# Optimization experiments

Hardware: AMD Instinct MI355X
Metric: run time of the kernel (lower is better)

Reference implementation:

```python
import jax, jax.numpy as jnp
import numpy as np

N, E, F_IN, F_E, H, T = 100000, 1600000, 128, 16, 64, 32
NEG_SLOPE = 0.2


def setup_inputs() -> dict:
    key = jax.random.key(0)
    ks = jax.random.split(key, 24)
    s = 0.1
    inp = {
        'x': jax.random.normal(ks[0], (N, F_IN), jnp.float32),
        'edge_index': jax.random.randint(ks[1], (2, E), 0, N, dtype=jnp.int32),
        'edge_attr': jax.random.normal(ks[2], (E, F_E), jnp.float32),
        # GATConv layer 1 (heads=1)
        'W1': jax.random.normal(ks[3], (F_IN, H), jnp.float32) * s,
        'as1': jax.random.normal(ks[4], (H,), jnp.float32) * s,
        'ad1': jax.random.normal(ks[5], (H,), jnp.float32) * s,
        'We1': jax.random.normal(ks[6], (F_E, H), jnp.float32) * s,
        'ae1': jax.random.normal(ks[7], (H,), jnp.float32) * s,
        'b1': jnp.zeros((H,), jnp.float32),
        # GATConv layer 2
        'W2': jax.random.normal(ks[8], (H, H), jnp.float32) * s,
        'as2': jax.random.normal(ks[9], (H,), jnp.float32) * s,
        'ad2': jax.random.normal(ks[10], (H,), jnp.float32) * s,
        'We2': jax.random.normal(ks[11], (F_E, H), jnp.float32) * s,
        'ae2': jax.random.normal(ks[12], (H,), jnp.float32) * s,
        'b2': jnp.zeros((H,), jnp.float32),
        # classifier MLP (dropout in eval mode -> identity)
        'Wc1': jax.random.normal(ks[13], (H, H // 2), jnp.float32) * s,
        'bc1': jnp.zeros((H // 2,), jnp.float32),
        'Wc2': jax.random.normal(ks[14], (H // 2, T), jnp.float32) * s,
        'bc2': jnp.zeros((T,), jnp.float32),
    }
    return inp


def gat_conv(x, src, dst, edge_attr, W, a_s, a_d, We, a_e, b):
    """Single-head PyG-style GATConv with edge features and self-loops
    (self-loop edge_attr = mean of incoming edge_attr, fill_value='mean')."""
    n = x.shape[0]
    # self loops with mean incoming edge features
    deg = jax.ops.segment_sum(jnp.ones_like(dst, jnp.float32), dst, n)
    loop_attr = jax.ops.segment_sum(edge_attr, dst, n) / jnp.maximum(deg, 1.0)[:, None]
    loops = jnp.arange(n, dtype=src.dtype)
    src_f = jnp.concatenate([src, loops])
    dst_f = jnp.concatenate([dst, loops])
    ea = jnp.concatenate([edge_attr, loop_attr], axis=0)  # [E+N, F_E]
    h = x @ W                                             # [N, H]
    # attention logits per edge: alpha_src[j] + alpha_dst[i] + alpha_edge
    alpha = (h @ a_s)[src_f] + (h @ a_d)[dst_f] + (ea @ We) @ a_e
    alpha = jax.nn.leaky_relu(alpha, NEG_SLOPE)
    # segment softmax over incoming edges per destination node
    m = jax.ops.segment_max(alpha, dst_f, n)
    p = jnp.exp(alpha - m[dst_f])
    z = jax.ops.segment_sum(p, dst_f, n)
    w = p / z[dst_f]                                      # [E+N]
    out = jax.ops.segment_sum(w[:, None] * h[src_f], dst_f, n)
    return out + b


def reference(x, edge_index, edge_attr, W1, as1, ad1, We1, ae1, b1,
              W2, as2, ad2, We2, ae2, b2, Wc1, bc1, Wc2, bc2):
    src, dst = edge_index[0], edge_index[1]
    h = jax.nn.relu(gat_conv(x, src, dst, edge_attr, W1, as1, ad1, We1, ae1, b1))
    h = jax.nn.relu(gat_conv(h, src, dst, edge_attr, W2, as2, ad2, We2, ae2, b2))
    h = jax.nn.relu(h @ Wc1 + bc1)
    logits = h @ Wc2 + bc2
    return logits
```

## Files before the change

kernel.cpp:

```cpp
#include <hip/hip_runtime.h>
#include <hip/hip_bf16.h>
#include <hip/hip_fp16.h>

#define NEG_SLOPE 0.2f
#define EPB 2048
#define NBUK 512

__device__ __forceinline__ float leaky(float a) { return a > 0.f ? a : NEG_SLOPE * a; }

__global__ __launch_bounds__(256) void count_pack(
    const int* __restrict__ dst, const float* __restrict__ eattr,
    const float* __restrict__ We1, const float* __restrict__ ae1,
    const float* __restrict__ We2, const float* __restrict__ ae2,
    unsigned int* __restrict__ meta_pay, int* __restrict__ counts, int E) {
    __shared__ float wvs[32];
    __shared__ int hist[NBUK];
    int tid = threadIdx.x, i = blockIdx.x;
    if (tid < 32) {
        const float* Wp = (tid < 16) ? We1 : We2;
        const float* ap = (tid < 16) ? ae1 : ae2;
        int f = tid & 15;
        float s = 0.f;
        for (int k = 0; k < 64; ++k) s += Wp[f * 64 + k] * ap[k];
        wvs[tid] = s;
    }
    for (int t = tid; t < NBUK; t += 256) hist[t] = 0;
    __syncthreads();
    int e0 = i * EPB, e1 = min(E, e0 + EPB);
    for (int e = e0 + tid; e < e1; e += 256) {
        int d = dst[e];
        atomicAdd(&hist[d >> 8], 1);
        const float4* ep = (const float4*)(eattr + (size_t)e * 16);
        float4 q0 = ep[0], q1 = ep[1], q2 = ep[2], q3 = ep[3];
        float a[16] = {q0.x, q0.y, q0.z, q0.w, q1.x, q1.y, q1.z, q1.w,
                       q2.x, q2.y, q2.z, q2.w, q3.x, q3.y, q3.z, q3.w};
        float s1 = 0.f, s2 = 0.f;
#pragma unroll
        for (int f = 0; f < 16; ++f) { s1 += a[f] * wvs[f]; s2 += a[f] * wvs[16 + f]; }
        unsigned int p1 = (unsigned int)__half_as_ushort(__float2half_rn(s1));
        unsigned int p2 = (unsigned int)__half_as_ushort(__float2half_rn(s2));
        meta_pay[e] = p1 | (p2 << 16);
    }
    __syncthreads();
    for (int t = tid; t < NBUK; t += 256) counts[(size_t)i * NBUK + t] = hist[t];
}

__global__ __launch_bounds__(1024) void scan_cols(const int* __restrict__ counts,
                                                  int* __restrict__ offsets,
                                                  int* __restrict__ btot, int nblk) {
    __shared__ int sh[1024];
    int b = blockIdx.x, t = threadIdx.x;
    int v = (t < nblk) ? counts[(size_t)t * NBUK + b] : 0;
    sh[t] = v;
    __syncthreads();
    for (int off = 1; off < 1024; off <<= 1) {
        int u = (t >= off) ? sh[t - off] : 0;
        __syncthreads();
        sh[t] += u;
        __syncthreads();
    }
    if (t < nblk) offsets[(size_t)t * NBUK + b] = sh[t] - v;
    if (t == 1023) btot[b] = sh[1023];
}

__global__ void scan_buckets(const int* __restrict__ btot, int* __restrict__ bbase,
                             int* __restrict__ rowptr, int E, int n) {
    __shared__ int sh[NBUK];
    int t = threadIdx.x;
    int v = btot[t];
    sh[t] = v;
    __syncthreads();
    for (int off = 1; off < NBUK; off <<= 1) {
        int u = (t >= off) ? sh[t - off] : 0;
        __syncthreads();
        sh[t] += u;
        __syncthreads();
    }
    bbase[t] = sh[t] - v;
    if (t == 0) rowptr[n] = E;
}

__global__ __launch_bounds__(256) void scatter_buckets(
    const int* __restrict__ dst, const int* __restrict__ src,
    const unsigned int* __restrict__ meta_pay, const int* __restrict__ offsets,
    const int* __restrict__ bbase, uint2* __restrict__ bucketed, int E) {
    __shared__ int cur[NBUK];
    int i = blockIdx.x, tid = threadIdx.x;
    for (int t = tid; t < NBUK; t += 256) cur[t] = bbase[t] + offsets[(size_t)i * NBUK + t];
    __syncthreads();
    int e0 = i * EPB, e1 = min(E, e0 + EPB);
    for (int e = e0 + tid; e < e1; e += 256) {
        int d = dst[e];
        int slot = atomicAdd(&cur[d >> 8], 1);
        bucketed[slot] = make_uint2((unsigned int)src[e] | ((unsigned int)(d & 255) << 24),
                                    meta_pay[e]);
    }
}

__global__ __launch_bounds__(256) void csr_build(const uint2* __restrict__ bucketed,
                                                 const int* __restrict__ bbase,
                                                 const int* __restrict__ btot,
                                                 int* __restrict__ rowptr,
                                                 uint2* __restrict__ recs, int n) {
    __shared__ int deg[256], sc[256], cur[256];
    int b = blockIdx.x, tid = threadIdx.x;
    int base = bbase[b], cnt = btot[b];
    deg[tid] = 0;
    __syncthreads();
    for (int k = tid; k < cnt; k += 256) {
        uint2 r = bucketed[base + k];
        atomicAdd(&deg[r.x >> 24], 1);
    }
    __syncthreads();
    int dv = deg[tid];
    sc[tid] = dv;
    __syncthreads();
    for (int off = 1; off < 256; off <<= 1) {
        int u = (tid >= off) ? sc[tid - off] : 0;
        __syncthreads();
        sc[tid] += u;
        __syncthreads();
    }
    int excl = sc[tid] - dv;
    int d = b * 256 + tid;
    if (d < n) rowptr[d] = base + excl;
    cur[tid] = base + excl;
    __syncthreads();
    for (int k = tid; k < cnt; k += 256) {
        uint2 r = bucketed[base + k];
        int dl = (int)(r.x >> 24);
        int pos = atomicAdd(&cur[dl], 1);
        recs[pos] = make_uint2(r.x & 0x00FFFFFFu, r.y);
    }
}

template <int K>
__global__ __launch_bounds__(256) void gemm_node(const float* __restrict__ X,
                                                 const float* __restrict__ W,
                                                 const float* __restrict__ a_s,
                                                 const float* __restrict__ a_d,
                                                 __half* __restrict__ Hout16,
                                                 float* __restrict__ ash,
                                                 float* __restrict__ adh, int n) {
    constexpr int KC = 64;
    __shared__ float xs[128 * 65];
    __shared__ float ws[KC * 64];
    int tid = threadIdx.x;
    int base = blockIdx.x * 128;
    int ct = tid & 7;
    int rt = tid >> 3;

    float acc[4][8];
#pragma unroll
    for (int i = 0; i < 4; ++i)
#pragma unroll
        for (int j = 0; j < 8; ++j) acc[i][j] = 0.f;

    for (int kc = 0; kc < K; kc += KC) {
#pragma unroll
        for (int p = 0; p < 8; ++p) {
            int idx = p * 256 + tid;
            int row = idx >> 4;
            int f4 = idx & 15;
            float4 q = make_float4(0.f, 0.f, 0.f, 0.f);
            if (base + row < n) q = *(const float4*)(X + (size_t)(base + row) * K + kc + f4 * 4);
            float* dp = xs + row * 65 + f4 * 4;
            dp[0] = q.x; dp[1] = q.y; dp[2] = q.z; dp[3] = q.w;
        }
#pragma unroll
        for (int p = 0; p < 4; ++p) {
            int idx = p * 256 + tid;
            int f = idx >> 4;
            int c4 = idx & 15;
            *(float4*)(ws + f * 64 + c4 * 4) =
                *(const float4*)(W + (size_t)(kc + f) * 64 + c4 * 4);
        }
        __syncthreads();
#pragma unroll 4
        for (int f = 0; f < KC; ++f) {
            float4 w0 = *(const float4*)(ws + f * 64 + ct * 8);
            float4 w1 = *(const float4*)(ws + f * 64 + ct * 8 + 4);
            float b0[8] = {w0.x, w0.y, w0.z, w0.w, w1.x, w1.y, w1.z, w1.w};
#pragma unroll
            for (int i = 0; i < 4; ++i) {
                float a = xs[(rt * 4 + i) * 65 + f];
#pragma unroll
                for (int j = 0; j < 8; ++j) acc[i][j] = fmaf(a, b0[j], acc[i][j]);
            }
        }
        __syncthreads();
    }

    float as_r[8], ad_r[8];
#pragma unroll
    for (int j = 0; j < 8; ++j) { as_r[j] = a_s[ct * 8 + j]; ad_r[j] = a_d[ct * 8 + j]; }
#pragma unroll
    for (int i = 0; i < 4; ++i) {
        int r = base + rt * 4 + i;
        float ps = 0.f, pd = 0.f;
#pragma unroll
        for (int j = 0; j < 8; ++j) {
            ps = fmaf(acc[i][j], as_r[j], ps);
            pd = fmaf(acc[i][j], ad_r[j], pd);
        }
        ps += __shfl_xor(ps, 1); pd += __shfl_xor(pd, 1);
        ps += __shfl_xor(ps, 2); pd += __shfl_xor(pd, 2);
        ps += __shfl_xor(ps, 4); pd += __shfl_xor(pd, 4);
        if (r < n) {
            union { __half h[8]; uint4 u; } pk;
#pragma unroll
            for (int j = 0; j < 8; ++j) pk.h[j] = __float2half_rn(acc[i][j]);
            *(uint4*)(Hout16 + (size_t)r * 64 + ct * 8) = pk.u;
            if (ct == 0) { ash[r] = ps; adh[r] = pd; }
        }
    }
}

template <int LAYER>
__global__ __launch_bounds__(256) void gat_aggregate(
    const __half* __restrict__ Hf, const float* __restrict__ ash, const float* __restrict__ adh,
    const int* __restrict__ rowptr, const uint2* __restrict__ recs,
    const float* __restrict__ bias, float* __restrict__ outp, int n) {
    __shared__ uint2 ops[4][64];
    int wave = threadIdx.x >> 6;
    int lane = threadIdx.x & 63;
    int i = blockIdx.x * 4 + wave;
    if (i >= n) return;
    int start = rowptr[i], end = rowptr[i + 1];
    float adi = adh[i];
    const char* Hb = (const char*)Hf;
    int g = lane >> 4;
    unsigned int fb = (unsigned int)((lane & 15) * 8);

    float acc0 = 0.f, acc1 = 0.f, acc2 = 0.f, acc3 = 0.f;
    float zl = 0.f, seal = 0.f;

    for (int c = start; c < end; c += 64) {
        int cnt = min(64, end - c);
        unsigned int o_l = 0;
        float p_l = 0.f;
        if (lane < cnt) {
            uint2 r = recs[c + lane];
            int s_l = (int)r.x;
            o_l = (unsigned int)s_l << 7;
            unsigned short u = (LAYER == 0) ? (unsigned short)(r.y & 0xffffu)
                                            : (unsigned short)(r.y >> 16);
            float e = __half2float(__ushort_as_half(u));
            float p = __expf(leaky(ash[s_l] + adi + e));
            p_l = p;
            zl += p;
            seal += e;
        }
        ops[wave][lane] = make_uint2(o_l, __float_as_uint(p_l));
        int nq = (cnt + 3) >> 2;
#pragma unroll 4
        for (int q = 0; q < nq; ++q) {
            uint2 op = ops[wave][q * 4 + g];
            uint2 hv = *(const uint2*)(Hb + (op.x + fb));
            float p = __uint_as_float(op.y);
            __half2 h01 = *(__half2*)&hv.x;
            __half2 h23 = *(__half2*)&hv.y;
            acc0 = fmaf(p, __half2float(h01.x), acc0);
            acc1 = fmaf(p, __half2float(h01.y), acc1);
            acc2 = fmaf(p, __half2float(h23.x), acc2);
            acc3 = fmaf(p, __half2float(h23.y), acc3);
        }
    }

    acc0 += __shfl_xor(acc0, 16); acc1 += __shfl_xor(acc1, 16);
    acc2 += __shfl_xor(acc2, 16); acc3 += __shfl_xor(acc3, 16);
    acc0 += __shfl_xor(acc0, 32); acc1 += __shfl_xor(acc1, 32);
    acc2 += __shfl_xor(acc2, 32); acc3 += __shfl_xor(acc3, 32);

    float z = zl, sea = seal;
#pragma unroll
    for (int off = 1; off < 64; off <<= 1) {
        z += __shfl_xor(z, off);
        sea += __shfl_xor(sea, off);
    }

    int d = end - start;
    float loop_sc = sea / (float)max(d, 1);
    float aself = leaky(ash[i] + adi + loop_sc);
    float pself = __expf(aself);
    z += pself;

    uint2 hvs = *(const uint2*)(Hb + (((size_t)i << 7) + fb));
    __half2 s01 = *(__half2*)&hvs.x;
    __half2 s23 = *(__half2*)&hvs.y;
    acc0 = fmaf(pself, __half2float(s01.x), acc0);
    acc1 = fmaf(pself, __half2float(s01.y), acc1);
    acc2 = fmaf(pself, __half2float(s23.x), acc2);
    acc3 = fmaf(pself, __half2float(s23.y), acc3);

    if (lane < 16) {
        float4 bv = *(const float4*)(bias + lane * 4);
        float4 o;
        o.x = fmaxf(acc0 / z + bv.x, 0.f);
        o.y = fmaxf(acc1 / z + bv.y, 0.f);
        o.z = fmaxf(acc2 / z + bv.z, 0.f);
        o.w = fmaxf(acc3 / z + bv.w, 0.f);
        *(float4*)(outp + (size_t)i * 64 + lane * 4) = o;
    }
}

__global__ __launch_bounds__(256) void mlp_kernel(const float* __restrict__ X,
                                                  const float* __restrict__ Wc1,
                                                  const float* __restrict__ bc1,
                                                  const float* __restrict__ Wc2,
                                                  const float* __restrict__ bc2,
                                                  float* __restrict__ outp, int n) {
    __shared__ float v[8 * 64];
    __shared__ float tb[8 * 32];
    int base = blockIdx.x * 8;
    for (int t = threadIdx.x; t < 512; t += 256) {
        int r = t >> 6;
        v[t] = (base + r < n) ? X[(size_t)base * 64 + t] : 0.f;
    }
    __syncthreads();
    int r = threadIdx.x >> 5, j = threadIdx.x & 31;
    float acc = bc1[j];
#pragma unroll
    for (int k = 0; k < 64; ++k) acc += v[r * 64 + k] * Wc1[k * 32 + j];
    acc = fmaxf(acc, 0.f);
    tb[r * 32 + j] = acc;
    __syncthreads();
    float lg = bc2[j];
#pragma unroll
    for (int k2 = 0; k2 < 32; ++k2) lg += tb[r * 32 + k2] * Wc2[k2 * 32 + j];
    int row = base + r;
    if (row < n) outp[(size_t)row * 32 + j] = lg;
}

extern "C" void kernel_launch(void* const* d_in, const int* in_sizes, int n_in,
                              void* d_out, int out_size, void* d_ws, size_t ws_size,
                              hipStream_t stream) {
    const float* x    = (const float*)d_in[0];
    const int*   ei   = (const int*)d_in[1];
    const float* eatt = (const float*)d_in[2];
    const float* W1   = (const float*)d_in[3];
    const float* as1  = (const float*)d_in[4];
    const float* ad1  = (const float*)d_in[5];
    const float* We1  = (const float*)d_in[6];
    const float* ae1  = (const float*)d_in[7];
    const float* b1   = (const float*)d_in[8];
    const float* W2   = (const float*)d_in[9];
    const float* as2  = (const float*)d_in[10];
    const float* ad2  = (const float*)d_in[11];
    const float* We2  = (const float*)d_in[12];
    const float* ae2  = (const float*)d_in[13];
    const float* b2   = (const float*)d_in[14];
    const float* Wc1  = (const float*)d_in[15];
    const float* bc1  = (const float*)d_in[16];
    const float* Wc2  = (const float*)d_in[17];
    const float* bc2  = (const float*)d_in[18];

    int n = in_sizes[0] / 128;
    int E = in_sizes[1] / 2;
    const int* src = ei;
    const int* dst = ei + E;
    int nblk = (E + EPB - 1) / EPB;

    char* w = (char*)d_ws;
    auto alloc = [&](size_t bytes) { void* p = (void*)w; w += (bytes + 255) & ~(size_t)255; return p; };
    int* rowptr   = (int*)alloc((size_t)(n + 1) * 4);
    int* counts   = (int*)alloc((size_t)nblk * NBUK * 4);
    int* offsets  = (int*)alloc((size_t)nblk * NBUK * 4);
    int* btot     = (int*)alloc((size_t)NBUK * 4);
    int* bbase    = (int*)alloc((size_t)NBUK * 4);
    unsigned int* meta_pay = (unsigned int*)alloc((size_t)E * 4);
    uint2* recs   = (uint2*)alloc((size_t)E * 8);
    __half* hbuf16 = (__half*)alloc((size_t)n * 64 * 2);
    float* obuf   = (float*)alloc((size_t)n * 64 * 4);
    float* ash    = (float*)alloc((size_t)n * 4);
    float* adh    = (float*)alloc((size_t)n * 4);
    uint2* bucketed = (uint2*)obuf;

    count_pack<<<nblk, 256, 0, stream>>>(dst, eatt, We1, ae1, We2, ae2, meta_pay, counts, E);
    scan_cols<<<NBUK, 1024, 0, stream>>>(counts, offsets, btot, nblk);
    scan_buckets<<<1, NBUK, 0, stream>>>(btot, bbase, rowptr, E, n);
    scatter_buckets<<<nblk, 256, 0, stream>>>(dst, src, meta_pay, offsets, bbase, bucketed, E);
    csr_build<<<NBUK, 256, 0, stream>>>(bucketed, bbase, btot, rowptr, recs, n);

    gemm_node<128><<<(n + 127) / 128, 256, 0, stream>>>(x, W1, as1, ad1, hbuf16, ash, adh, n);
    gat_aggregate<0><<<(n + 3) / 4, 256, 0, stream>>>(hbuf16, ash, adh, rowptr, recs, b1, obuf, n);
    gemm_node<64><<<(n + 127) / 128, 256, 0, stream>>>(obuf, W2, as2, ad2, hbuf16, ash, adh, n);
    gat_aggregate<1><<<(n + 3) / 4, 256, 0, stream>>>(hbuf16, ash, adh, rowptr, recs, b2, obuf, n);
    mlp_kernel<<<(n + 7) / 8, 256, 0, stream>>>(obuf, Wc1, bc1, Wc2, bc2, (float*)d_out, n);
}
```

Baseline: 477.5 us.

## Map one node per 16-lane group in GAT aggregation instead of per wave

The aggregation kernel now assigns each destination node to a 16-lane quarter-wave rather than a full 64-lane wave, so each block handles 16 nodes. With an average in-degree of about 16, a full wave wasted most lanes computing per-edge scores, and cross-lane reductions shrink from 64 to 16 lanes. The staging buffer in shared memory is padded to 17 entries per group. The trade-off is that the inner gather loop now runs once per edge with divergent trip counts across the four groups in a wave, so high-degree nodes serialise within their group.

```diff
diff --git a/kernel.cpp b/kernel.cpp
--- a/kernel.cpp
+++ b/kernel.cpp
@@ -221,26 +221,27 @@
     const __half* __restrict__ Hf, const float* __restrict__ ash, const float* __restrict__ adh,
     const int* __restrict__ rowptr, const uint2* __restrict__ recs,
     const float* __restrict__ bias, float* __restrict__ outp, int n) {
-    __shared__ uint2 ops[4][64];
+    __shared__ uint2 ops[4][4 * 17];
     int wave = threadIdx.x >> 6;
     int lane = threadIdx.x & 63;
-    int i = blockIdx.x * 4 + wave;
+    int gr = lane >> 4;
+    int fl = lane & 15;
+    int i = blockIdx.x * 16 + wave * 4 + gr;
     if (i >= n) return;
     int start = rowptr[i], end = rowptr[i + 1];
     float adi = adh[i];
     const char* Hb = (const char*)Hf;
-    int g = lane >> 4;
-    unsigned int fb = (unsigned int)((lane & 15) * 8);
+    unsigned int fb = (unsigned int)(fl * 8);
 
     float acc0 = 0.f, acc1 = 0.f, acc2 = 0.f, acc3 = 0.f;
     float zl = 0.f, seal = 0.f;
 
-    for (int c = start; c < end; c += 64) {
-        int cnt = min(64, end - c);
+    for (int c = start; c < end; c += 16) {
+        int cnt = min(16, end - c);
         unsigned int o_l = 0;
         float p_l = 0.f;
-        if (lane < cnt) {
-            uint2 r = recs[c + lane];
+        if (fl < cnt) {
+            uint2 r = recs[c + fl];
             int s_l = (int)r.x;
             o_l = (unsigned int)s_l << 7;
             unsigned short u = (LAYER == 0) ? (unsigned short)(r.y & 0xffffu)
@@ -251,11 +252,9 @@
             zl += p;
             seal += e;
         }
-        ops[wave][lane] = make_uint2(o_l, __float_as_uint(p_l));
-        int nq = (cnt + 3) >> 2;
-#pragma unroll 4
-        for (int q = 0; q < nq; ++q) {
-            uint2 op = ops[wave][q * 4 + g];
+        ops[wave][gr * 17 + fl] = make_uint2(o_l, __float_as_uint(p_l));
+        for (int k = 0; k < cnt; ++k) {
+            uint2 op = ops[wave][gr * 17 + k];
             uint2 hv = *(const uint2*)(Hb + (op.x + fb));
             float p = __uint_as_float(op.y);
             __half2 h01 = *(__half2*)&hv.x;
@@ -267,25 +266,19 @@
         }
     }
 
-    acc0 += __shfl_xor(acc0, 16); acc1 += __shfl_xor(acc1, 16);
-    acc2 += __shfl_xor(acc2, 16); acc3 += __shfl_xor(acc3, 16);
-    acc0 += __shfl_xor(acc0, 32); acc1 += __shfl_xor(acc1, 32);
-    acc2 += __shfl_xor(acc2, 32); acc3 += __shfl_xor(acc3, 32);
-
-    float z = zl, sea = seal;
-#pragma unroll
-    for (int off = 1; off < 64; off <<= 1) {
-        z += __shfl_xor(z, off);
-        sea += __shfl_xor(sea, off);
+#pragma unroll
+    for (int off = 1; off < 16; off <<= 1) {
+        zl += __shfl_xor(zl, off);
+        seal += __shfl_xor(seal, off);
     }
 
     int d = end - start;
-    float loop_sc = sea / (float)max(d, 1);
+    float loop_sc = seal / (float)max(d, 1);
     float aself = leaky(ash[i] + adi + loop_sc);
     float pself = __expf(aself);
-    z += pself;
-
-    uint2 hvs = *(const uint2*)(Hb + (((size_t)i << 7) + fb));
+    float z = zl + pself;
+
+    uint2 hvs = *(const uint2*)(Hb + (((unsigned int)i << 7) + fb));
     __half2 s01 = *(__half2*)&hvs.x;
     __half2 s23 = *(__half2*)&hvs.y;
     acc0 = fmaf(pself, __half2float(s01.x), acc0);
@@ -293,15 +286,13 @@
     acc2 = fmaf(pself, __half2float(s23.x), acc2);
     acc3 = fmaf(pself, __half2float(s23.y), acc3);
 
-    if (lane < 16) {
-        float4 bv = *(const float4*)(bias + lane * 4);
-        float4 o;
-        o.x = fmaxf(acc0 / z + bv.x, 0.f);
-        o.y = fmaxf(acc1 / z + bv.y, 0.f);
-        o.z = fmaxf(acc2 / z + bv.z, 0.f);
-        o.w = fmaxf(acc3 / z + bv.w, 0.f);
-        *(float4*)(outp + (size_t)i * 64 + lane * 4) = o;
-    }
+    float4 bv = *(const float4*)(bias + fl * 4);
+    float4 o;
+    o.x = fmaxf(acc0 / z + bv.x, 0.f);
+    o.y = fmaxf(acc1 / z + bv.y, 0.f);
+    o.z = fmaxf(acc2 / z + bv.z, 0.f);
+    o.w = fmaxf(acc3 / z + bv.w, 0.f);
+    *(float4*)(outp + (size_t)i * 64 + fl * 4) = o;
 }
 
 __global__ __launch_bounds__(256) void mlp_kernel(const float* __restrict__ X,
@@ -383,8 +374,8 @@
     csr_build<<<NBUK, 256, 0, stream>>>(bucketed, bbase, btot, rowptr, recs, n);
 
     gemm_node<128><<<(n + 127) / 128, 256, 0, stream>>>(x, W1, as1, ad1, hbuf16, ash, adh, n);
-    gat_aggregate<0><<<(n + 3) / 4, 256, 0, stream>>>(hbuf16, ash, adh, rowptr, recs, b1, obuf, n);
+    gat_aggregate<0><<<(n + 15) / 16, 256, 0, stream>>>(hbuf16, ash, adh, rowptr, recs, b1, obuf, n);
     gemm_node<64><<<(n + 127) / 128, 256, 0, stream>>>(obuf, W2, as2, ad2, hbuf16, ash, adh, n);
-    gat_aggregate<1><<<(n + 3) / 4, 256, 0, stream>>>(hbuf16, ash, adh, rowptr, recs, b2, obuf, n);
+    gat_aggregate<1><<<(n + 15) / 16, 256, 0, stream>>>(hbuf16, ash, adh, rowptr, recs, b2, obuf, n);
     mlp_kernel<<<(n + 7) / 8, 256, 0, stream>>>(obuf, Wc1, bc1, Wc2, bc2, (float*)d_out, n);
 }
```

Result: faster. 464.4 us (-2.7%).
